# Kernel tuning notes

Hardware: AMD Instinct MI355X
Metric: run time of the kernel (lower is better)

The kernel has to match this reference:

```python
import jax, jax.numpy as jnp
import numpy as np

B, D, NH, HD = 32, 384, 8, 48
HP = WP = 14
N = HP * WP
L = 24
EPS_LN = 1e-5


def _ln(x, w, b):
    m = jnp.mean(x, -1, keepdims=True)
    v = jnp.mean((x - m) ** 2, -1, keepdims=True)
    return (x - m) * jax.lax.rsqrt(v + EPS_LN) * w + b


def _gelu(x):
    return jax.nn.gelu(x, approximate=False)


def _conv(x, w, s, p, groups=1):
    return jax.lax.conv_general_dilated(x, w, (s, s), [(p, p), (p, p)],
        dimension_numbers=('NCHW', 'OIHW', 'NCHW'), feature_group_count=groups)


def _bn(x, g, b):
    # eval-mode BatchNorm2d with running_mean=0, running_var=1
    scale = g * jax.lax.rsqrt(jnp.asarray(1.0 + 1e-5, x.dtype))
    return x * scale[None, :, None, None] + b[None, :, None, None]


def _pos_embed(pos_w, pos_b):
    two_pi = 2.0 * np.pi
    y = (jnp.arange(HP, dtype=jnp.float32) + 1.0) / ((HP + 1e-6) * two_pi)
    xg = (jnp.arange(WP, dtype=jnp.float32) + 1.0) / ((WP + 1e-6) * two_pi)
    y_embed = jnp.broadcast_to(y[:, None], (HP, WP))
    x_embed = jnp.broadcast_to(xg[None, :], (HP, WP))
    dim_t = 10000.0 ** (2.0 * (jnp.arange(32) // 2).astype(jnp.float32) / 32.0)
    px = x_embed[..., None] / dim_t  # [H,W,32]
    py = y_embed[..., None] / dim_t
    px = jnp.stack([jnp.sin(px[..., 0::2]), jnp.cos(px[..., 1::2])], -1).reshape(HP, WP, 32)
    py = jnp.stack([jnp.sin(py[..., 0::2]), jnp.cos(py[..., 1::2])], -1).reshape(HP, WP, 32)
    pos = jnp.concatenate([py, px], -1)  # [H,W,64]
    pos = jnp.einsum('hwc,dc->hwd', pos, pos_w[:, :, 0, 0]) + pos_b
    return pos.reshape(1, N, D)


def _xca_block(t, p):
    Bc = t.shape[0]
    h = _ln(t, p['n1_w'], p['n1_b'])
    qkv = (h @ p['qkv_w'].T + p['qkv_b']).reshape(Bc, N, 3, NH, HD)
    q = qkv[:, :, 0].transpose(0, 2, 3, 1)  # [B,H,d,N]
    k = qkv[:, :, 1].transpose(0, 2, 3, 1)
    v = qkv[:, :, 2].transpose(0, 2, 3, 1)
    q = q / jnp.maximum(jnp.linalg.norm(q, axis=-1, keepdims=True), 1e-12)
    k = k / jnp.maximum(jnp.linalg.norm(k, axis=-1, keepdims=True), 1e-12)
    attn = jnp.einsum('bhdn,bhen->bhde', q, k) * p['temp'][None, :, None, None]
    a = jax.nn.softmax(attn, -1)  # channel-wise softmax over d_h
    o = jnp.einsum('bhde,bhen->bnhd', a, v).reshape(Bc, N, D)
    o = o @ p['proj_w'].T + p['proj_b']
    t = t + p['g1'] * o
    h = _ln(t, p['n3_w'], p['n3_b']).transpose(0, 2, 1).reshape(Bc, D, HP, WP)
    h = _conv(h, p['lpi1_w'], 1, 1, groups=D) + p['lpi1_b'][None, :, None, None]
    h = _bn(_gelu(h), p['lpi_bn_g'], p['lpi_bn_b'])
    h = _conv(h, p['lpi2_w'], 1, 1, groups=D) + p['lpi2_b'][None, :, None, None]
    t = t + p['g3'] * h.reshape(Bc, D, N).transpose(0, 2, 1)
    h = _ln(t, p['n2_w'], p['n2_b'])
    h = _gelu(h @ p['fc1_w'].T + p['fc1_b']) @ p['fc2_w'].T + p['fc2_b']
    return t + p['g2'] * h


def _ca_block(t, p):
    Bc, Nc, _ = t.shape
    h = _ln(t, p['n1_w'], p['n1_b'])
    qkv = (h @ p['qkv_w'].T + p['qkv_b']).reshape(Bc, Nc, 3, NH, HD)
    q = qkv[:, :, 0].transpose(0, 2, 1, 3)  # [B,H,N,d]
    k = qkv[:, :, 1].transpose(0, 2, 1, 3)
    v = qkv[:, :, 2].transpose(0, 2, 1, 3)
    attn = jnp.sum(q[:, :, :1] * k, -1) * (HD ** -0.5)  # [B,H,N]
    a = jax.nn.softmax(attn, -1)
    cls = jnp.einsum('bhn,bhnd->bhd', a, v).reshape(Bc, 1, D)
    cls = cls @ p['proj_w'].T + p['proj_b']
    attn_out = jnp.concatenate([cls, h[:, 1:]], 1)
    t = t + p['g1'] * attn_out
    t = _ln(t, p['n2_w'], p['n2_b'])
    res = t
    cls2 = _gelu(t[:, :1] @ p['fc1_w'].T + p['fc1_b']) @ p['fc2_w'].T + p['fc2_b']
    return jnp.concatenate([p['g2'] * cls2, t[:, 1:]], 1) + res


def setup_inputs() -> dict:
    key = jax.random.key(0)
    k = iter(jax.random.split(key, 64))
    def rn(shape, std=0.02):
        return jax.random.normal(next(k), shape, jnp.float32) * std
    inp = {}
    inp['x'] = jax.random.normal(next(k), (B, 3, 224, 224), jnp.float32)
    inp['cls_token'] = rn((1, 1, D))
    inp['pos_w'] = rn((D, 64, 1, 1))
    inp['pos_b'] = jnp.zeros((D,))
    for i, (co, ci) in enumerate([(48, 3), (96, 48), (192, 96), (384, 192)], 1):
        inp['pe_w%d' % i] = rn((co, ci, 3, 3))
        inp['pe_g%d' % i] = jnp.ones((co,))
        inp['pe_b%d' % i] = jnp.zeros((co,))
    inp['xqkv_w'] = rn((L, 3 * D, D)); inp['xqkv_b'] = jnp.zeros((L, 3 * D))
    inp['xproj_w'] = rn((L, D, D)); inp['xproj_b'] = jnp.zeros((L, D))
    inp['xtemp'] = jnp.ones((L, NH))
    for n in ('n1', 'n2', 'n3'):
        inp['x%s_w' % n] = jnp.ones((L, D)); inp['x%s_b' % n] = jnp.zeros((L, D))
    inp['xfc1_w'] = rn((L, 4 * D, D)); inp['xfc1_b'] = jnp.zeros((L, 4 * D))
    inp['xfc2_w'] = rn((L, D, 4 * D)); inp['xfc2_b'] = jnp.zeros((L, D))
    inp['xlpi1_w'] = rn((L, D, 1, 3, 3), 0.1); inp['xlpi1_b'] = jnp.zeros((L, D))
    inp['xlpi2_w'] = rn((L, D, 1, 3, 3), 0.1); inp['xlpi2_b'] = jnp.zeros((L, D))
    inp['xbn_g'] = jnp.ones((L, D)); inp['xbn_b'] = jnp.zeros((L, D))
    for g in ('g1', 'g2', 'g3'):
        inp['x%s' % g] = jnp.full((L, D), 1e-5)
    L2 = 2
    inp['cqkv_w'] = rn((L2, 3 * D, D)); inp['cqkv_b'] = jnp.zeros((L2, 3 * D))
    inp['cproj_w'] = rn((L2, D, D)); inp['cproj_b'] = jnp.zeros((L2, D))
    for n in ('n1', 'n2'):
        inp['c%s_w' % n] = jnp.ones((L2, D)); inp['c%s_b' % n] = jnp.zeros((L2, D))
    inp['cfc1_w'] = rn((L2, 4 * D, D)); inp['cfc1_b'] = jnp.zeros((L2, 4 * D))
    inp['cfc2_w'] = rn((L2, D, 4 * D)); inp['cfc2_b'] = jnp.zeros((L2, D))
    inp['cg1'] = jnp.full((L2, D), 1e-5); inp['cg2'] = jnp.full((L2, D), 1e-5)
    inp['norm_w'] = jnp.ones((D,)); inp['norm_b'] = jnp.zeros((D,))
    inp['head_w'] = rn((1000, D)); inp['head_b'] = jnp.zeros((1000,))
    return inp


def reference(x, cls_token, pos_w, pos_b, pe_w1, pe_g1, pe_b1, pe_w2, pe_g2, pe_b2, pe_w3, pe_g3, pe_b3, pe_w4, pe_g4, pe_b4, xqkv_w, xqkv_b, xproj_w, xproj_b, xtemp, xn1_w, xn1_b, xn2_w, xn2_b, xn3_w, xn3_b, xfc1_w, xfc1_b, xfc2_w, xfc2_b, xlpi1_w, xlpi1_b, xlpi2_w, xlpi2_b, xbn_g, xbn_b, xg1, xg2, xg3, cqkv_w, cqkv_b, cproj_w, cproj_b, cn1_w, cn1_b, cn2_w, cn2_b, cfc1_w, cfc1_b, cfc2_w, cfc2_b, cg1, cg2, norm_w, norm_b, head_w, head_b):
    h = _gelu(_bn(_conv(x, pe_w1, 2, 1), pe_g1, pe_b1))
    h = _gelu(_bn(_conv(h, pe_w2, 2, 1), pe_g2, pe_b2))
    h = _gelu(_bn(_conv(h, pe_w3, 2, 1), pe_g3, pe_b3))
    h = _bn(_conv(h, pe_w4, 2, 1), pe_g4, pe_b4)  # [B,D,14,14]
    t = h.reshape(h.shape[0], D, N).transpose(0, 2, 1)  # [B,N,D]
    t = t + _pos_embed(pos_w, pos_b)
    xca = {'qkv_w': xqkv_w, 'qkv_b': xqkv_b, 'proj_w': xproj_w, 'proj_b': xproj_b,
           'temp': xtemp, 'n1_w': xn1_w, 'n1_b': xn1_b, 'n2_w': xn2_w, 'n2_b': xn2_b,
           'n3_w': xn3_w, 'n3_b': xn3_b, 'fc1_w': xfc1_w, 'fc1_b': xfc1_b,
           'fc2_w': xfc2_w, 'fc2_b': xfc2_b, 'lpi1_w': xlpi1_w, 'lpi1_b': xlpi1_b,
           'lpi2_w': xlpi2_w, 'lpi2_b': xlpi2_b, 'lpi_bn_g': xbn_g, 'lpi_bn_b': xbn_b,
           'g1': xg1, 'g2': xg2, 'g3': xg3}
    t, _ = jax.lax.scan(lambda c, p: (_xca_block(c, p), None), t, xca)
    t = jnp.concatenate([jnp.broadcast_to(cls_token, (t.shape[0], 1, D)), t], 1)
    for i in range(2):
        p = {'qkv_w': cqkv_w[i], 'qkv_b': cqkv_b[i], 'proj_w': cproj_w[i],
             'proj_b': cproj_b[i], 'n1_w': cn1_w[i], 'n1_b': cn1_b[i],
             'n2_w': cn2_w[i], 'n2_b': cn2_b[i], 'fc1_w': cfc1_w[i],
             'fc1_b': cfc1_b[i], 'fc2_w': cfc2_w[i], 'fc2_b': cfc2_b[i],
             'g1': cg1[i], 'g2': cg2[i]}
        t = _ca_block(t, p)
    t = _ln(t, norm_w, norm_b)[:, 0]
    return t @ head_w.T + head_b
```

## Files before the change

kernel.cpp:

```cpp
#include <hip/hip_runtime.h>
#include <hip/hip_bf16.h>

#define B_ 32
#define D_ 384
#define N_ 196
#define NH_ 8
#define HD_ 48
#define L_ 24

typedef __bf16 bf16x8 __attribute__((ext_vector_type(8)));
typedef float f32x4 __attribute__((ext_vector_type(4)));

__device__ __forceinline__ float gelu_f(float v){
    return 0.5f * v * (1.0f + erff(v * 0.70710678118654752f));
}

__global__ __launch_bounds__(256) void cvt_bf(const float* __restrict__ s, __bf16* __restrict__ d, long n){
    long i = ((long)blockIdx.x * 256 + threadIdx.x) * 8;
    if (i >= n) return;
    float4 a = *reinterpret_cast<const float4*>(s + i);
    float4 b = *reinterpret_cast<const float4*>(s + i + 4);
    bf16x8 r;
    r[0] = (__bf16)a.x; r[1] = (__bf16)a.y; r[2] = (__bf16)a.z; r[3] = (__bf16)a.w;
    r[4] = (__bf16)b.x; r[5] = (__bf16)b.y; r[6] = (__bf16)b.z; r[7] = (__bf16)b.w;
    *reinterpret_cast<bf16x8*>(d + i) = r;
}

__global__ __launch_bounds__(256) void cvt_pad(const float* __restrict__ s, __bf16* __restrict__ d,
                                               int rows, int K, int rows_pad){
    int id = blockIdx.x * 256 + threadIdx.x;
    if (id >= rows_pad * K) return;
    int r = id / K;
    d[id] = (r < rows) ? (__bf16)s[id] : (__bf16)0.f;
}

__global__ __launch_bounds__(256) void wprep(const float* __restrict__ w, __bf16* __restrict__ W2,
                                             int Co, int Ci, int Kpad){
    int id = blockIdx.x * 256 + threadIdx.x;
    if (id >= Co * Kpad) return;
    int co = id / Kpad, k = id - co * Kpad;
    float v = 0.f;
    if (k < 9 * Ci){
        int tap = k / Ci, ci = k - tap * Ci;
        v = w[((long)co * Ci + ci) * 9 + tap];
    }
    W2[id] = (__bf16)v;
}

__global__ __launch_bounds__(256) void im2col_x(const float* __restrict__ x, __bf16* __restrict__ A){
    int id = blockIdx.x * 256 + threadIdx.x;
    if (id >= 401408) return;
    int ox = id % 112; int t1 = id / 112; int oy = t1 % 112; int b = t1 / 112;
    __bf16 buf[32];
    #pragma unroll
    for (int i = 0; i < 32; i++) buf[i] = (__bf16)0.f;
    const float* xb = x + (long)b * 3 * 224 * 224;
    #pragma unroll
    for (int tap = 0; tap < 9; tap++){
        int ky = tap / 3, kx = tap % 3;
        int iy = oy * 2 - 1 + ky, ix = ox * 2 - 1 + kx;
        if ((unsigned)iy < 224u && (unsigned)ix < 224u){
            #pragma unroll
            for (int ci = 0; ci < 3; ci++)
                buf[tap * 3 + ci] = (__bf16)xb[((long)ci * 224 + iy) * 224 + ix];
        }
    }
    __bf16* dst = A + (long)id * 32;
    #pragma unroll
    for (int i = 0; i < 4; i++)
        *reinterpret_cast<bf16x8*>(dst + i * 8) = *reinterpret_cast<bf16x8*>(buf + i * 8);
}

__global__ __launch_bounds__(256) void im2col_bf(const __bf16* __restrict__ in, __bf16* __restrict__ A,
                                                 int C, int Hi, int Wi, int Ho, int Wo, int Kpad, int total){
    int id = blockIdx.x * 256 + threadIdx.x;
    if (id >= total) return;
    int tap = id % 9; int pix = id / 9;
    int ox = pix % Wo; int t1 = pix / Wo; int oy = t1 % Ho; int b = t1 / Ho;
    int ky = tap / 3, kx = tap % 3;
    int iy = oy * 2 - 1 + ky, ix = ox * 2 - 1 + kx;
    __bf16* dst = A + (long)pix * Kpad + tap * C;
    if ((unsigned)iy < (unsigned)Hi && (unsigned)ix < (unsigned)Wi){
        const __bf16* src = in + ((long)(b * Hi + iy) * Wi + ix) * C;
        for (int c = 0; c < C; c += 8)
            *reinterpret_cast<bf16x8*>(dst + c) = *reinterpret_cast<const bf16x8*>(src + c);
    } else {
        bf16x8 z{};
        for (int c = 0; c < C; c += 8) *reinterpret_cast<bf16x8*>(dst + c) = z;
    }
    if (tap == 0){
        bf16x8 z{};
        for (int c = 9 * C; c < Kpad; c += 8)
            *reinterpret_cast<bf16x8*>(A + (long)pix * Kpad + c) = z;
    }
}

template<int GELU, int POSOUT>
__global__ __launch_bounds__(256) void gemm_conv(const __bf16* __restrict__ A, int Kpad,
                                                 const __bf16* __restrict__ W,
                                                 const float* __restrict__ g, const float* __restrict__ bb,
                                                 void* __restrict__ Cv, int N,
                                                 const float* __restrict__ pos){
    __shared__ __align__(16) char smem[20480];
    char* Ab = smem;
    char* Bb = smem + 10240;
    const int tid  = threadIdx.x;
    const int lane = tid & 63;
    const int wn   = (tid >> 6) & 1;
    const int wm   = tid >> 7;
    const int row0 = blockIdx.x * 128;
    const int col0 = blockIdx.y * 128;
    const int hi = lane >> 4, lo = lane & 15;
    f32x4 acc[4][4] = {};
    auto loadA = [&](int kk, int i)->bf16x8 {
        int p = i * 256 + tid;
        int r = p >> 2, cq = p & 3;
        return *reinterpret_cast<const bf16x8*>(A + (long)(row0 + r) * Kpad + kk + cq * 8);
    };
    auto loadB = [&](int kk, int i)->bf16x8 {
        int p = i * 256 + tid;
        int r = p >> 2, cq = p & 3;
        int gc = col0 + r;
        bf16x8 vw{};
        if (gc < N) vw = *reinterpret_cast<const bf16x8*>(W + (long)gc * Kpad + kk + cq * 8);
        return vw;
    };
    bf16x8 vaC0 = loadA(0, 0), vaC1 = loadA(0, 1);
    bf16x8 vwC0 = loadB(0, 0), vwC1 = loadB(0, 1);
    for (int k0 = 0; k0 < Kpad; k0 += 32){
        #pragma unroll
        for (int i = 0; i < 2; i++){
            int p = i * 256 + tid;
            int r = p >> 2, cq = p & 3;
            *reinterpret_cast<bf16x8*>(Ab + r * 80 + cq * 16) = i ? vaC1 : vaC0;
            *reinterpret_cast<bf16x8*>(Bb + r * 80 + cq * 16) = i ? vwC1 : vwC0;
        }
        __syncthreads();
        int kn = (k0 + 32 < Kpad) ? k0 + 32 : k0;
        bf16x8 vaN0 = loadA(kn, 0), vaN1 = loadA(kn, 1);
        bf16x8 vwN0 = loadB(kn, 0), vwN1 = loadB(kn, 1);
        bf16x8 af[4], bfr[4];
        #pragma unroll
        for (int m = 0; m < 4; m++)
            af[m] = *reinterpret_cast<const bf16x8*>(Ab + (wm * 64 + m * 16 + lo) * 80 + hi * 16);
        #pragma unroll
        for (int n = 0; n < 4; n++)
            bfr[n] = *reinterpret_cast<const bf16x8*>(Bb + (wn * 64 + n * 16 + lo) * 80 + hi * 16);
        #pragma unroll
        for (int m = 0; m < 4; m++)
            #pragma unroll
            for (int n = 0; n < 4; n++)
                acc[m][n] = __builtin_amdgcn_mfma_f32_16x16x32_bf16(af[m], bfr[n], acc[m][n], 0, 0, 0);
        __syncthreads();
        vaC0 = vaN0; vaC1 = vaN1; vwC0 = vwN0; vwC1 = vwN1;
    }
    float* Cf = (float*)Cv;
    __bf16* Cb = (__bf16*)Cv;
    #pragma unroll
    for (int m = 0; m < 4; m++){
        #pragma unroll
        for (int n = 0; n < 4; n++){
            int row = row0 + wm * 64 + m * 16 + hi * 4;
            int col = col0 + wn * 64 + n * 16 + lo;
            if (col >= N) continue;
            float scale = g[col] * rsqrtf(1.0f + 1e-5f);
            float bv = bb[col];
            #pragma unroll
            for (int j = 0; j < 4; j++){
                float v = acc[m][n][j] * scale + bv;
                if (GELU) v = gelu_f(v);
                if (POSOUT)
                    Cf[(long)(row + j) * 384 + col] = v + pos[((row + j) % 196) * 384 + col];
                else
                    Cb[(long)(row + j) * N + col] = (__bf16)v;
            }
        }
    }
}

__global__ __launch_bounds__(128) void ln384(const float* __restrict__ x, long xstride,
                                             const float* __restrict__ w, const float* __restrict__ b,
                                             float* __restrict__ y, long ystride){
    long row = blockIdx.x;
    int tid = threadIdx.x;
    const float* xr = x + row * xstride;
    float v0 = xr[tid], v1 = xr[tid + 128], v2 = xr[tid + 256];
    float s = v0 + v1 + v2;
    float ss = v0 * v0 + v1 * v1 + v2 * v2;
    for (int off = 32; off; off >>= 1){ s += __shfl_down(s, off); ss += __shfl_down(ss, off); }
    __shared__ float rs[2], rss[2];
    if ((tid & 63) == 0){ rs[tid >> 6] = s; rss[tid >> 6] = ss; }
    __syncthreads();
    float S = rs[0] + rs[1], SS = rss[0] + rss[1];
    float m = S * (1.0f / 384.0f);
    float var = SS * (1.0f / 384.0f) - m * m;
    float r = rsqrtf(var + 1e-5f);
    float* yr = y + row * ystride;
    yr[tid]       = (v0 - m) * r * w[tid]       + b[tid];
    yr[tid + 128] = (v1 - m) * r * w[tid + 128] + b[tid + 128];
    yr[tid + 256] = (v2 - m) * r * w[tid + 256] + b[tid + 256];
}

__global__ __launch_bounds__(128) void ln384_bf(const float* __restrict__ x,
                                                const float* __restrict__ w, const float* __restrict__ b,
                                                __bf16* __restrict__ y){
    long row = blockIdx.x;
    int tid = threadIdx.x;
    const float* xr = x + row * 384;
    float v0 = xr[tid], v1 = xr[tid + 128], v2 = xr[tid + 256];
    float s = v0 + v1 + v2;
    float ss = v0 * v0 + v1 * v1 + v2 * v2;
    for (int off = 32; off; off >>= 1){ s += __shfl_down(s, off); ss += __shfl_down(ss, off); }
    __shared__ float rs[2], rss[2];
    if ((tid & 63) == 0){ rs[tid >> 6] = s; rss[tid >> 6] = ss; }
    __syncthreads();
    float S = rs[0] + rs[1], SS = rss[0] + rss[1];
    float m = S * (1.0f / 384.0f);
    float var = SS * (1.0f / 384.0f) - m * m;
    float r = rsqrtf(var + 1e-5f);
    __bf16* yr = y + row * 384;
    yr[tid]       = (__bf16)((v0 - m) * r * w[tid]       + b[tid]);
    yr[tid + 128] = (__bf16)((v1 - m) * r * w[tid + 128] + b[tid + 128]);
    yr[tid + 256] = (__bf16)((v2 - m) * r * w[tid + 256] + b[tid + 256]);
}

__global__ __launch_bounds__(128) void proj_red_lnt(const float* __restrict__ pp,
                                                    const float* __restrict__ pbias,
                                                    const float* __restrict__ g1,
                                                    float* __restrict__ t,
                                                    const float* __restrict__ n3w, const float* __restrict__ n3b,
                                                    float* __restrict__ ht){
    long row = blockIdx.x;
    int tid = threadIdx.x;
    const long MT = 6272L * 384;
    float v[3];
    #pragma unroll
    for (int i = 0; i < 3; i++){
        int c = tid + i * 128;
        long idx = row * 384 + c;
        float sacc = pp[idx] + pp[MT + idx] + pbias[c];
        v[i] = t[idx] + g1[c] * sacc;
        t[idx] = v[i];
    }
    float s = v[0] + v[1] + v[2];
    float ss = v[0] * v[0] + v[1] * v[1] + v[2] * v[2];
    for (int off = 32; off; off >>= 1){ s += __shfl_down(s, off); ss += __shfl_down(ss, off); }
    __shared__ float rs[2], rss[2];
    if ((tid & 63) == 0){ rs[tid >> 6] = s; rss[tid >> 6] = ss; }
    __syncthreads();
    float S = rs[0] + rs[1], SS = rss[0] + rss[1];
    float m = S * (1.0f / 384.0f);
    float var = SS * (1.0f / 384.0f) - m * m;
    float r = rsqrtf(var + 1e-5f);
    int b = (int)(row / 196), n = (int)(row % 196);
    float* yb = ht + ((long)b * 384) * 196 + n;
    #pragma unroll
    for (int i = 0; i < 3; i++){
        int c = tid + i * 128;
        yb[(long)c * 196] = (v[i] - m) * r * n3w[c] + n3b[c];
    }
}

__global__ __launch_bounds__(128) void fc2_red_ln(const float* __restrict__ pp,
                                                  const float* __restrict__ fbias,
                                                  const float* __restrict__ g2,
                                                  float* __restrict__ t,
                                                  const float* __restrict__ n1w, const float* __restrict__ n1b,
                                                  __bf16* __restrict__ h){
    long row = blockIdx.x;
    int tid = threadIdx.x;
    const long MT = 6272L * 384;
    float v[3];
    #pragma unroll
    for (int i = 0; i < 3; i++){
        int c = tid + i * 128;
        long idx = row * 384 + c;
        float sacc = pp[idx] + pp[MT + idx] + pp[2 * MT + idx] + fbias[c];
        v[i] = t[idx] + g2[c] * sacc;
        t[idx] = v[i];
    }
    float s = v[0] + v[1] + v[2];
    float ss = v[0] * v[0] + v[1] * v[1] + v[2] * v[2];
    for (int off = 32; off; off >>= 1){ s += __shfl_down(s, off); ss += __shfl_down(ss, off); }
    __shared__ float rs[2], rss[2];
    if ((tid & 63) == 0){ rs[tid >> 6] = s; rss[tid >> 6] = ss; }
    __syncthreads();
    float S = rs[0] + rs[1], SS = rss[0] + rss[1];
    float m = S * (1.0f / 384.0f);
    float var = SS * (1.0f / 384.0f) - m * m;
    float r = rsqrtf(var + 1e-5f);
    __bf16* yr = h + row * 384;
    #pragma unroll
    for (int i = 0; i < 3; i++){
        int c = tid + i * 128;
        yr[c] = (__bf16)((v[i] - m) * r * n1w[c] + n1b[c]);
    }
}

template<int MODE, int OUTBF, int ACVT, int GUARD, int SPLITK, int NGUARD>
__global__ __launch_bounds__(256) void gemm_bb2(const void* __restrict__ Av, long lda,
                                                const __bf16* __restrict__ W, int Kw,
                                                const float* __restrict__ bias,
                                                void* __restrict__ Cv, long ldc,
                                                int K, int M, int Ncols){
    __shared__ __align__(16) char smem[15360];
    char* Ab = smem;
    char* Bb = smem + 5120;
    const int tid = threadIdx.x;
    const int lane = tid & 63;
    const int wn = tid >> 6;
    const int row0 = blockIdx.x * 64;
    const int col0 = blockIdx.y * 128;
    const int hi = lane >> 4, lo = lane & 15;
    const int kbase = SPLITK ? blockIdx.z * K : 0;
    const __bf16* Abf = (const __bf16*)Av;
    const float* Af = (const float*)Av;
    const int r_a = tid >> 2, cq_a = tid & 3;
    f32x4 acc[4][2] = {};
    auto loadA = [&](int kk)->bf16x8 {
        bf16x8 va{};
        int grow = row0 + r_a;
        if (!GUARD || grow < M){
            long ai = (long)grow * lda + kk + cq_a * 8;
            if (ACVT){
                float4 a0 = *reinterpret_cast<const float4*>(Af + ai);
                float4 a1 = *reinterpret_cast<const float4*>(Af + ai + 4);
                va[0] = (__bf16)a0.x; va[1] = (__bf16)a0.y; va[2] = (__bf16)a0.z; va[3] = (__bf16)a0.w;
                va[4] = (__bf16)a1.x; va[5] = (__bf16)a1.y; va[6] = (__bf16)a1.z; va[7] = (__bf16)a1.w;
            } else {
                va = *reinterpret_cast<const bf16x8*>(Abf + ai);
            }
        }
        return va;
    };
    auto loadB = [&](int kk, int i)->bf16x8 {
        int p = i * 256 + tid;
        int r = p >> 2, cq = p & 3;
        return *reinterpret_cast<const bf16x8*>(W + (long)(col0 + r) * Kw + kk + cq * 8);
    };
    bf16x8 vaC = loadA(kbase);
    bf16x8 vwC0 = loadB(kbase, 0), vwC1 = loadB(kbase, 1);
    for (int k0 = 0; k0 < K; k0 += 32){
        *reinterpret_cast<bf16x8*>(Ab + r_a * 80 + cq_a * 16) = vaC;
        #pragma unroll
        for (int i = 0; i < 2; i++){
            int p = i * 256 + tid;
            int r = p >> 2, cq = p & 3;
            *reinterpret_cast<bf16x8*>(Bb + r * 80 + cq * 16) = i ? vwC1 : vwC0;
        }
        __syncthreads();
        int kn = kbase + ((k0 + 32 < K) ? k0 + 32 : k0);
        bf16x8 vaN = loadA(kn);
        bf16x8 vwN0 = loadB(kn, 0), vwN1 = loadB(kn, 1);
        bf16x8 af[4], bfr[2];
        #pragma unroll
        for (int m = 0; m < 4; m++)
            af[m] = *reinterpret_cast<const bf16x8*>(Ab + (m * 16 + lo) * 80 + hi * 16);
        #pragma unroll
        for (int n = 0; n < 2; n++)
            bfr[n] = *reinterpret_cast<const bf16x8*>(Bb + (wn * 32 + n * 16 + lo) * 80 + hi * 16);
        #pragma unroll
        for (int m = 0; m < 4; m++)
            #pragma unroll
            for (int n = 0; n < 2; n++)
                acc[m][n] = __builtin_amdgcn_mfma_f32_16x16x32_bf16(af[m], bfr[n], acc[m][n], 0, 0, 0);
        __syncthreads();
        vaC = vaN; vwC0 = vwN0; vwC1 = vwN1;
    }
    float* Cf = (float*)Cv;
    __bf16* Cb = (__bf16*)Cv;
    if (SPLITK) Cf += (long)blockIdx.z * M * ldc;
    #pragma unroll
    for (int m = 0; m < 4; m++){
        #pragma unroll
        for (int n = 0; n < 2; n++){
            int row = row0 + m * 16 + hi * 4;
            int col = col0 + wn * 32 + n * 16 + lo;
            if (NGUARD && col >= Ncols) continue;
            float bv = (MODE == 3) ? 0.f : bias[col];
            #pragma unroll
            for (int j = 0; j < 4; j++){
                if (GUARD && (row + j) >= M) continue;
                float v = acc[m][n][j] + bv;
                if (MODE == 1) v = gelu_f(v);
                long ci = (long)(row + j) * ldc + col;
                if (OUTBF) Cb[ci] = (__bf16)v;
                else Cf[ci] = v;
            }
        }
    }
}

__global__ __launch_bounds__(384) void pos_embed(const float* __restrict__ pw, const float* __restrict__ pb,
                                                 float* __restrict__ pos){
    __shared__ float p64[64];
    int n = blockIdx.x;
    int iy = n / 14, ix = n % 14;
    int t = threadIdx.x;
    if (t < 64){
        int axis = t >> 5;
        int c = t & 31;
        int u = c >> 1;
        float coord = (axis == 0) ? (float)(iy + 1) : (float)(ix + 1);
        float val = coord / ((14.0f + 1e-6f) * 6.283185307179586f);
        float T = powf(10000.0f, (float)u / 16.0f);
        float a = val / T;
        p64[t] = (c & 1) ? cosf(a) : sinf(a);
    }
    __syncthreads();
    float acc = 0.f;
    const float* wr = pw + (long)t * 64;
    #pragma unroll 8
    for (int c = 0; c < 64; c++) acc += p64[c] * wr[c];
    pos[n * 384 + t] = acc + pb[t];
}

__global__ __launch_bounds__(256) void xca2(const __bf16* __restrict__ qkv, const float* __restrict__ temp,
                                            __bf16* __restrict__ o){
    __shared__ __align__(16) char smem[74880];
    __bf16* qs = (__bf16*)smem;
    __bf16* ks = (__bf16*)(smem + 22272);
    __bf16* vt = (__bf16*)(smem + 44544);
    float* inq = (float*)(smem + 74496);
    float* ink = (float*)(smem + 74688);
    float* att = (float*)smem;
    __bf16* abf = (__bf16*)(smem + 22272);
    int bh = blockIdx.x;
    int b = bh >> 3, h = bh & 7;
    const int tid = threadIdx.x;
    const int wid = tid >> 6, lane = tid & 63;
    const int hi = lane >> 4, lo = lane & 15;
    const __bf16* base = qkv + ((long)b * 196) * 1152 + h * 48;
    bf16x8 z8 = {};
    for (int idx = tid; idx < 48 * 28; idx += 256){
        int d = idx / 28, n = 196 + idx % 28;
        qs[d * 232 + n] = (__bf16)0.f;
        ks[d * 232 + n] = (__bf16)0.f;
    }
    for (int idx = tid; idx < 208 * 2; idx += 256){
        int n = idx >> 1, c = 48 + (idx & 1) * 8;
        *reinterpret_cast<bf16x8*>(vt + n * 72 + c) = z8;
    }
    for (int ch = tid; ch < 196 * 6; ch += 256){
        int n = ch / 6, c = ch % 6, d0 = c * 8;
        bf16x8 q8 = *reinterpret_cast<const bf16x8*>(base + (long)n * 1152 + d0);
        bf16x8 k8 = *reinterpret_cast<const bf16x8*>(base + (long)n * 1152 + 384 + d0);
        #pragma unroll
        for (int j = 0; j < 8; j++){
            qs[(d0 + j) * 232 + n] = q8[j];
            ks[(d0 + j) * 232 + n] = k8[j];
        }
        bf16x8 v8 = *reinterpret_cast<const bf16x8*>(base + (long)n * 1152 + 768 + d0);
        *reinterpret_cast<bf16x8*>(vt + n * 72 + d0) = v8;
    }
    __syncthreads();
    for (int r = wid; r < 48; r += 4){
        float sq = 0.f, sk = 0.f;
        for (int n = lane; n < 196; n += 64){
            float qv = (float)qs[r * 232 + n];
            float kv = (float)ks[r * 232 + n];
            sq += qv * qv; sk += kv * kv;
        }
        for (int off = 32; off; off >>= 1){ sq += __shfl_down(sq, off); sk += __shfl_down(sk, off); }
        if (lane == 0){
            inq[r] = 1.0f / fmaxf(sqrtf(sq), 1e-12f);
            ink[r] = 1.0f / fmaxf(sqrtf(sk), 1e-12f);
        }
    }
    __syncthreads();
    float tempv = temp[h];
    f32x4 qk0 = {}, qk1 = {}, qk2 = {};
    __builtin_amdgcn_s_setprio(1);
    {
        int mi = wid / 3, ni = wid % 3;
        #pragma unroll
        for (int k0 = 0; k0 < 224; k0 += 32){
            bf16x8 af = *reinterpret_cast<const bf16x8*>(qs + (mi * 16 + lo) * 232 + k0 + hi * 8);
            bf16x8 bf = *reinterpret_cast<const bf16x8*>(ks + (ni * 16 + lo) * 232 + k0 + hi * 8);
            qk0 = __builtin_amdgcn_mfma_f32_16x16x32_bf16(af, bf, qk0, 0, 0, 0);
        }
    }
    {
        int tt = wid + 4;
        int mi = tt / 3, ni = tt % 3;
        #pragma unroll
        for (int k0 = 0; k0 < 224; k0 += 32){
            bf16x8 af = *reinterpret_cast<const bf16x8*>(qs + (mi * 16 + lo) * 232 + k0 + hi * 8);
            bf16x8 bf = *reinterpret_cast<const bf16x8*>(ks + (ni * 16 + lo) * 232 + k0 + hi * 8);
            qk1 = __builtin_amdgcn_mfma_f32_16x16x32_bf16(af, bf, qk1, 0, 0, 0);
        }
    }
    if (wid == 0){
        int mi = 2, ni = 2;
        #pragma unroll
        for (int k0 = 0; k0 < 224; k0 += 32){
            bf16x8 af = *reinterpret_cast<const bf16x8*>(qs + (mi * 16 + lo) * 232 + k0 + hi * 8);
            bf16x8 bf = *reinterpret_cast<const bf16x8*>(ks + (ni * 16 + lo) * 232 + k0 + hi * 8);
            qk2 = __builtin_amdgcn_mfma_f32_16x16x32_bf16(af, bf, qk2, 0, 0, 0);
        }
    }
    __builtin_amdgcn_s_setprio(0);
    __syncthreads();
    {
        int mi = wid / 3, ni = wid % 3;
        int e = ni * 16 + lo;
        float se = ink[e] * tempv;
        #pragma unroll
        for (int j = 0; j < 4; j++){
            int d = mi * 16 + hi * 4 + j;
            att[d * 68 + e] = qk0[j] * inq[d] * se;
        }
    }
    {
        int tt = wid + 4;
        int mi = tt / 3, ni = tt % 3;
        int e = ni * 16 + lo;
        float se = ink[e] * tempv;
        #pragma unroll
        for (int j = 0; j < 4; j++){
            int d = mi * 16 + hi * 4 + j;
            att[d * 68 + e] = qk1[j] * inq[d] * se;
        }
    }
    if (wid == 0){
        int e = 2 * 16 + lo;
        float se = ink[e] * tempv;
        #pragma unroll
        for (int j = 0; j < 4; j++){
            int d = 2 * 16 + hi * 4 + j;
            att[d * 68 + e] = qk2[j] * inq[d] * se;
        }
    }
    __syncthreads();
    if (tid < 192){
        int r = tid >> 2, q4 = tid & 3;
        const float* row = att + r * 68 + q4 * 12;
        float mx = -1e30f;
        #pragma unroll
        for (int i = 0; i < 12; i++) mx = fmaxf(mx, row[i]);
        mx = fmaxf(mx, __shfl_xor(mx, 1));
        mx = fmaxf(mx, __shfl_xor(mx, 2));
        float pv[12]; float sm = 0.f;
        #pragma unroll
        for (int i = 0; i < 12; i++){ pv[i] = expf(row[i] - mx); sm += pv[i]; }
        sm += __shfl_xor(sm, 1);
        sm += __shfl_xor(sm, 2);
        float inv = 1.0f / sm;
        #pragma unroll
        for (int i = 0; i < 12; i++) abf[r * 72 + q4 * 12 + i] = (__bf16)(pv[i] * inv);
    }
    for (int idx = tid; idx < 48 * 3; idx += 256){
        int r = idx / 3, c = 48 + (idx % 3) * 8;
        *reinterpret_cast<bf16x8*>(abf + r * 72 + c) = z8;
    }
    __syncthreads();
    __bf16* ob = o + ((long)b * 196) * 384 + h * 48;
    __builtin_amdgcn_s_setprio(1);
    for (int tt = wid; tt < 39; tt += 4){
        int mi = tt / 13, ni = tt % 13;
        f32x4 acc = {};
        #pragma unroll
        for (int e0 = 0; e0 < 64; e0 += 32){
            bf16x8 af = *reinterpret_cast<const bf16x8*>(abf + (mi * 16 + lo) * 72 + e0 + hi * 8);
            bf16x8 bf = *reinterpret_cast<const bf16x8*>(vt + (ni * 16 + lo) * 72 + e0 + hi * 8);
            acc = __builtin_amdgcn_mfma_f32_16x16x32_bf16(af, bf, acc, 0, 0, 0);
        }
        int n = ni * 16 + lo;
        if (n < 196){
            #pragma unroll
            for (int j = 0; j < 4; j++){
                int d = mi * 16 + hi * 4 + j;
                ob[(long)n * 384 + d] = (__bf16)acc[j];
            }
        }
    }
    __builtin_amdgcn_s_setprio(0);
}

__global__ __launch_bounds__(256) void lpi(const float* __restrict__ ht,
                                           const float* __restrict__ w1, const float* __restrict__ b1,
                                           const float* __restrict__ bng, const float* __restrict__ bnb,
                                           const float* __restrict__ w2, const float* __restrict__ b2,
                                           const float* __restrict__ g3, float* __restrict__ t){
    int bd = blockIdx.x;
    int d = bd % 384, b = bd / 384;
    __shared__ float p[16][16];
    __shared__ float p2[16][16];
    __shared__ float wA[9], wB[9];
    int tt = threadIdx.x;
    int yy = tt / 16, xx = tt % 16;
    p[yy][xx] = 0.f; p2[yy][xx] = 0.f;
    if (tt < 9){ wA[tt] = w1[d * 9 + tt]; wB[tt] = w2[d * 9 + tt]; }
    __syncthreads();
    if (tt < 196){
        int y = tt / 14, x = tt % 14;
        p[y + 1][x + 1] = ht[((long)b * 384 + d) * 196 + tt];
    }
    __syncthreads();
    if (tt < 196){
        int y = tt / 14, x = tt % 14;
        float a = 0.f;
        #pragma unroll
        for (int ky = 0; ky < 3; ky++)
            #pragma unroll
            for (int kx = 0; kx < 3; kx++)
                a += wA[ky * 3 + kx] * p[y + ky][x + kx];
        a += b1[d];
        a = gelu_f(a);
        a = a * (bng[d] * rsqrtf(1.0f + 1e-5f)) + bnb[d];
        p2[y + 1][x + 1] = a;
    }
    __syncthreads();
    if (tt < 196){
        int y = tt / 14, x = tt % 14;
        float a = 0.f;
        #pragma unroll
        for (int ky = 0; ky < 3; ky++)
            #pragma unroll
            for (int kx = 0; kx < 3; kx++)
                a += wB[ky * 3 + kx] * p2[y + ky][x + kx];
        a += b2[d];
        long ti = ((long)b * 196 + tt) * 384 + d;
        t[ti] += g3[d] * a;
    }
}

__global__ __launch_bounds__(256) void concat_cls(const float* __restrict__ t, const float* __restrict__ clstok,
                                                  float* __restrict__ tc){
    long i = (long)blockIdx.x * 256 + threadIdx.x;
    if (i >= (long)B_ * 197 * 384) return;
    int d = (int)(i % 384);
    long bn = i / 384;
    int n = (int)(bn % 197);
    int b = (int)(bn / 197);
    tc[i] = (n == 0) ? clstok[d] : t[((long)b * 196 + (n - 1)) * 384 + d];
}

__global__ __launch_bounds__(256) void ca_attn(const __bf16* __restrict__ qkv, float* __restrict__ clsp){
    int bh = blockIdx.x;
    int b = bh >> 3, h = bh & 7;
    const __bf16* base = qkv + (long)b * 197 * 1152 + h * 48;
    __shared__ float q0[48];
    __shared__ float at2[197];
    __shared__ float smax, ssum;
    int tid = threadIdx.x;
    if (tid < 48) q0[tid] = (float)base[tid];
    __syncthreads();
    if (tid < 197){
        const __bf16* kr = base + (long)tid * 1152 + 384;
        float s = 0.f;
        for (int d = 0; d < 48; d++) s += q0[d] * (float)kr[d];
        at2[tid] = s * rsqrtf(48.0f);
    }
    __syncthreads();
    if (tid == 0){
        float m = -1e30f;
        for (int n = 0; n < 197; n++) m = fmaxf(m, at2[n]);
        smax = m;
    }
    __syncthreads();
    if (tid < 197) at2[tid] = expf(at2[tid] - smax);
    __syncthreads();
    if (tid == 0){
        float s = 0.f;
        for (int n = 0; n < 197; n++) s += at2[n];
        ssum = s;
    }
    __syncthreads();
    if (tid < 48){
        const __bf16* vb = base + 768 + tid;
        float s = 0.f;
        for (int n = 0; n < 197; n++) s += at2[n] * (float)vb[(long)n * 1152];
        clsp[b * 384 + h * 48 + tid] = s / ssum;
    }
}

__global__ __launch_bounds__(256) void ca_update1(const float* __restrict__ clso, const float* __restrict__ hc,
                                                  const float* __restrict__ g1, float* __restrict__ tc){
    long i = (long)blockIdx.x * 256 + threadIdx.x;
    if (i >= (long)B_ * 197 * 384) return;
    int d = (int)(i % 384);
    long bn = i / 384;
    int n = (int)(bn % 197);
    int b = (int)(bn / 197);
    float add = (n == 0) ? clso[b * 384 + d] : hc[i];
    tc[i] += g1[d] * add;
}

__global__ __launch_bounds__(256) void ca_update2(const float* __restrict__ cls2, const float* __restrict__ hc,
                                                  const float* __restrict__ g2, float* __restrict__ tc){
    long i = (long)blockIdx.x * 256 + threadIdx.x;
    if (i >= (long)B_ * 197 * 384) return;
    int d = (int)(i % 384);
    long bn = i / 384;
    int n = (int)(bn % 197);
    int b = (int)(bn / 197);
    float hv = hc[i];
    tc[i] = (n == 0) ? (g2[d] * cls2[b * 384 + d] + hv) : (hv + hv);
}

extern "C" void kernel_launch(void* const* d_in, const int* in_sizes, int n_in,
                              void* d_out, int out_size, void* d_ws, size_t ws_size,
                              hipStream_t stream){
    (void)in_sizes; (void)n_in; (void)out_size; (void)ws_size;
    const float* x      = (const float*)d_in[0];
    const float* clstok = (const float*)d_in[1];
    const float* pos_w  = (const float*)d_in[2];
    const float* pos_b  = (const float*)d_in[3];
    const float* pe_w[4] = {(const float*)d_in[4], (const float*)d_in[7], (const float*)d_in[10], (const float*)d_in[13]};
    const float* pe_g[4] = {(const float*)d_in[5], (const float*)d_in[8], (const float*)d_in[11], (const float*)d_in[14]};
    const float* pe_b[4] = {(const float*)d_in[6], (const float*)d_in[9], (const float*)d_in[12], (const float*)d_in[15]};
    const float* xqkv_w = (const float*)d_in[16];
    const float* xqkv_b = (const float*)d_in[17];
    const float* xproj_w = (const float*)d_in[18];
    const float* xproj_b = (const float*)d_in[19];
    const float* xtemp  = (const float*)d_in[20];
    const float* xn1_w = (const float*)d_in[21];
    const float* xn1_b = (const float*)d_in[22];
    const float* xn2_w = (const float*)d_in[23];
    const float* xn2_b = (const float*)d_in[24];
    const float* xn3_w = (const float*)d_in[25];
    const float* xn3_b = (const float*)d_in[26];
    const float* xfc1_w = (const float*)d_in[27];
    const float* xfc1_b = (const float*)d_in[28];
    const float* xfc2_w = (const float*)d_in[29];
    const float* xfc2_b = (const float*)d_in[30];
    const float* xlpi1_w = (const float*)d_in[31];
    const float* xlpi1_b = (const float*)d_in[32];
    const float* xlpi2_w = (const float*)d_in[33];
    const float* xlpi2_b = (const float*)d_in[34];
    const float* xbn_g = (const float*)d_in[35];
    const float* xbn_b = (const float*)d_in[36];
    const float* xg1 = (const float*)d_in[37];
    const float* xg2 = (const float*)d_in[38];
    const float* xg3 = (const float*)d_in[39];
    const float* cqkv_w = (const float*)d_in[40];
    const float* cqkv_b = (const float*)d_in[41];
    const float* cproj_w = (const float*)d_in[42];
    const float* cproj_b = (const float*)d_in[43];
    const float* cn1_w = (const float*)d_in[44];
    const float* cn1_b = (const float*)d_in[45];
    const float* cn2_w = (const float*)d_in[46];
    const float* cn2_b = (const float*)d_in[47];
    const float* cfc1_w = (const float*)d_in[48];
    const float* cfc1_b = (const float*)d_in[49];
    const float* cfc2_w = (const float*)d_in[50];
    const float* cfc2_b = (const float*)d_in[51];
    const float* cg1 = (const float*)d_in[52];
    const float* cg2 = (const float*)d_in[53];
    const float* norm_w = (const float*)d_in[54];
    const float* norm_b = (const float*)d_in[55];
    const float* head_w = (const float*)d_in[56];
    const float* head_b = (const float*)d_in[57];
    float* outp = (float*)d_out;

    float* ws = (float*)d_ws;
    __bf16* A1   = (__bf16*)(ws);
    __bf16* A2   = (__bf16*)(ws);
    __bf16* A3   = (__bf16*)(ws);
    __bf16* A4   = (__bf16*)(ws);
    __bf16* out1 = (__bf16*)(ws + 22500000L);
    __bf16* out2 = (__bf16*)(ws + 22500000L);
    __bf16* out3 = (__bf16*)(ws + 27400000L);
    __bf16* wcv  = (__bf16*)(ws + 36000000L);
    __bf16* W1c = wcv;
    __bf16* W2c = wcv + 1536;
    __bf16* W3c = wcv + 44544;
    __bf16* W4c = wcv + 216576;
    __bf16* wqkv_bf = (__bf16*)(ws);
    __bf16* wproj_bf = (__bf16*)(ws + 5308416L);
    __bf16* wfc1_bf = (__bf16*)(ws + 7077888L);
    __bf16* wfc2_bf = (__bf16*)(ws + 14155776L);
    float*  t       = ws + 21233664L;
    float*  pos     = ws + 23642112L;
    __bf16* h_bf    = (__bf16*)(ws + 23717376L);
    __bf16* qkv_bf  = (__bf16*)(ws + 24921600L);
    __bf16* o_bf    = (__bf16*)(ws + 28534272L);
    float*  ht      = ws + 29738496L;
    __bf16* f1_bf   = (__bf16*)(ws + 32146944L);
    float*  pproj   = ws + 32146944L;
    float*  pfc2    = ws + 24921600L;
    float* tc   = ws;
    float* hc   = ws + 2420736L;
    __bf16* qkvc_bf = (__bf16*)(ws + 4841472L);
    float* clsp = ws + 8472576L;
    float* clso = clsp + 12288;
    float* f1c  = clso + 12288;
    float* cls2 = f1c + 49152;
    float* clsf = cls2 + 12288;
    __bf16* cqkv_bf  = (__bf16*)(ws + 9000000L);
    __bf16* cproj_bf = (__bf16*)(ws + 9500000L);
    __bf16* cfc1_bf  = (__bf16*)(ws + 9800000L);
    __bf16* cfc2_bf  = (__bf16*)(ws + 10400000L);
    __bf16* headw_bf = (__bf16*)(ws + 11000000L);

    wprep<<<(48 * 32 + 255) / 256, 256, 0, stream>>>(pe_w[0], W1c, 48, 3, 32);
    wprep<<<(96 * 448 + 255) / 256, 256, 0, stream>>>(pe_w[1], W2c, 96, 48, 448);
    wprep<<<(192 * 896 + 255) / 256, 256, 0, stream>>>(pe_w[2], W3c, 192, 96, 896);
    wprep<<<(384 * 1728 + 255) / 256, 256, 0, stream>>>(pe_w[3], W4c, 384, 192, 1728);

    im2col_x<<<1568, 256, 0, stream>>>(x, A1);
    { dim3 g(3136, 1); gemm_conv<1, 0><<<g, 256, 0, stream>>>(A1, 32, W1c, pe_g[0], pe_b[0], out1, 48, nullptr); }
    im2col_bf<<<(100352 * 9 + 255) / 256, 256, 0, stream>>>(out1, A2, 48, 112, 112, 56, 56, 448, 100352 * 9);
    { dim3 g(784, 1); gemm_conv<1, 0><<<g, 256, 0, stream>>>(A2, 448, W2c, pe_g[1], pe_b[1], out2, 96, nullptr); }
    im2col_bf<<<(25088 * 9 + 255) / 256, 256, 0, stream>>>(out2, A3, 96, 56, 56, 28, 28, 896, 25088 * 9);
    pos_embed<<<196, 384, 0, stream>>>(pos_w, pos_b, pos);
    { dim3 g(196, 2); gemm_conv<1, 0><<<g, 256, 0, stream>>>(A3, 896, W3c, pe_g[2], pe_b[2], out3, 192, nullptr); }
    im2col_bf<<<(6272 * 9 + 255) / 256, 256, 0, stream>>>(out3, A4, 192, 28, 28, 14, 14, 1728, 6272 * 9);
    { dim3 g(49, 3); gemm_conv<0, 1><<<g, 256, 0, stream>>>(A4, 1728, W4c, pe_g[3], pe_b[3], t, 384, pos); }

    {
        long n1 = (long)L_ * 1152 * 384;
        long n2 = (long)L_ * 384 * 384;
        long n3 = (long)L_ * 1536 * 384;
        cvt_bf<<<(int)((n1 + 2047) / 2048), 256, 0, stream>>>(xqkv_w, wqkv_bf, n1);
        cvt_bf<<<(int)((n2 + 2047) / 2048), 256, 0, stream>>>(xproj_w, wproj_bf, n2);
        cvt_bf<<<(int)((n3 + 2047) / 2048), 256, 0, stream>>>(xfc1_w, wfc1_bf, n3);
        cvt_bf<<<(int)((n3 + 2047) / 2048), 256, 0, stream>>>(xfc2_w, wfc2_bf, n3);
    }

    const int M = B_ * N_;
    ln384_bf<<<M, 128, 0, stream>>>(t, xn1_w, xn1_b, h_bf);
    for (int l = 0; l < L_; l++){
        {
            dim3 g(98, 9);
            gemm_bb2<0, 1, 0, 0, 0, 0><<<g, 256, 0, stream>>>(h_bf, 384, wqkv_bf + (long)l * 1152 * 384, 384,
                                                              xqkv_b + l * 1152, qkv_bf, 1152, 384, M, 0);
        }
        xca2<<<B_ * NH_, 256, 0, stream>>>(qkv_bf, xtemp + l * 8, o_bf);
        {
            dim3 g(98, 3, 2);
            gemm_bb2<3, 0, 0, 0, 1, 0><<<g, 256, 0, stream>>>(o_bf, 384, wproj_bf + (long)l * 384 * 384, 384,
                                                              nullptr, pproj, 384, 192, M, 0);
        }
        proj_red_lnt<<<M, 128, 0, stream>>>(pproj, xproj_b + l * 384, xg1 + l * 384, t,
                                            xn3_w + l * 384, xn3_b + l * 384, ht);
        lpi<<<B_ * D_, 256, 0, stream>>>(ht, xlpi1_w + (long)l * 384 * 9, xlpi1_b + l * 384,
                                         xbn_g + l * 384, xbn_b + l * 384,
                                         xlpi2_w + (long)l * 384 * 9, xlpi2_b + l * 384,
                                         xg3 + l * 384, t);
        ln384_bf<<<M, 128, 0, stream>>>(t, xn2_w + l * 384, xn2_b + l * 384, h_bf);
        {
            dim3 g(98, 12);
            gemm_bb2<1, 1, 0, 0, 0, 0><<<g, 256, 0, stream>>>(h_bf, 384, wfc1_bf + (long)l * 1536 * 384, 384,
                                                              xfc1_b + l * 1536, f1_bf, 1536, 384, M, 0);
        }
        {
            dim3 g(98, 3, 3);
            gemm_bb2<3, 0, 0, 0, 1, 0><<<g, 256, 0, stream>>>(f1_bf, 1536, wfc2_bf + (long)l * 1536 * 384, 1536,
                                                              nullptr, pfc2, 384, 512, M, 0);
        }
        int ln = (l + 1) % L_;
        fc2_red_ln<<<M, 128, 0, stream>>>(pfc2, xfc2_b + l * 384, xg2 + l * 384, t,
                                          xn1_w + ln * 384, xn1_b + ln * 384, h_bf);
    }

    const long NC = (long)B_ * 197 * 384;
    concat_cls<<<(int)(NC / 256), 256, 0, stream>>>(t, clstok, tc);
    {
        long nc = (long)2 * 1152 * 384;
        cvt_bf<<<(int)((nc + 2047) / 2048), 256, 0, stream>>>(cqkv_w, cqkv_bf, nc);
        long np = (long)2 * 384 * 384;
        cvt_bf<<<(int)((np + 2047) / 2048), 256, 0, stream>>>(cproj_w, cproj_bf, np);
        long nf = (long)2 * 1536 * 384;
        cvt_bf<<<(int)((nf + 2047) / 2048), 256, 0, stream>>>(cfc1_w, cfc1_bf, nf);
        cvt_bf<<<(int)((nf + 2047) / 2048), 256, 0, stream>>>(cfc2_w, cfc2_bf, nf);
        cvt_pad<<<(1024 * 384 + 255) / 256, 256, 0, stream>>>(head_w, headw_bf, 1000, 384, 1024);
    }
    const int MC = B_ * 197;
    for (int i = 0; i < 2; i++){
        ln384<<<MC, 128, 0, stream>>>(tc, 384, cn1_w + i * 384, cn1_b + i * 384, hc, 384);
        {
            dim3 g(99, 9);
            gemm_bb2<0, 1, 1, 1, 0, 0><<<g, 256, 0, stream>>>(hc, 384, cqkv_bf + (long)i * 1152 * 384, 384,
                                                              cqkv_b + i * 1152, qkvc_bf, 1152, 384, MC, 0);
        }
        ca_attn<<<B_ * NH_, 256, 0, stream>>>(qkvc_bf, clsp);
        {
            dim3 g(1, 3);
            gemm_bb2<0, 0, 1, 1, 0, 0><<<g, 256, 0, stream>>>(clsp, 384, cproj_bf + (long)i * 384 * 384, 384,
                                                              cproj_b + i * 384, clso, 384, 384, 32, 0);
        }
        ca_update1<<<(int)(NC / 256), 256, 0, stream>>>(clso, hc, cg1 + i * 384, tc);
        ln384<<<MC, 128, 0, stream>>>(tc, 384, cn2_w + i * 384, cn2_b + i * 384, hc, 384);
        {
            dim3 g(1, 12);
            gemm_bb2<1, 0, 1, 1, 0, 0><<<g, 256, 0, stream>>>(hc, (long)197 * 384, cfc1_bf + (long)i * 1536 * 384, 384,
                                                              cfc1_b + i * 1536, f1c, 1536, 384, 32, 0);
        }
        {
            dim3 g(1, 3);
            gemm_bb2<0, 0, 1, 1, 0, 0><<<g, 256, 0, stream>>>(f1c, 1536, cfc2_bf + (long)i * 1536 * 384, 1536,
                                                              cfc2_b + i * 384, cls2, 384, 1536, 32, 0);
        }
        ca_update2<<<(int)(NC / 256), 256, 0, stream>>>(cls2, hc, cg2 + i * 384, tc);
    }

    ln384<<<32, 128, 0, stream>>>(tc, (long)197 * 384, norm_w, norm_b, clsf, 384);
    {
        dim3 g(1, 8);
        gemm_bb2<0, 0, 1, 1, 0, 1><<<g, 256, 0, stream>>>(clsf, 384, headw_bf, 384,
                                                          head_b, outp, 1000, 384, 32, 1000);
    }
}
```

Measured before the change: 4.589 ms.

## Replace split-K fp32 partials with 64x64 bf16 GEMM and bf16 residual buffers

Swaps the split-K proj and fc2 GEMMs, which wrote fp32 partial sums that a reduction kernel then combined, for a new small-tile 64x64 GEMM that runs the full K loop and writes bias-added bf16 output. The LPI kernel now writes its scaled output to a bf16 buffer instead of doing a read-modify-write on t. The separate LN kernel is replaced by a fused residual-add plus LN. This cuts fp32 partial-sum traffic and extra passes over memory, at the cost of bf16 rounding on the residual branch and less parallelism in K per GEMM block.

```diff
diff --git a/kernel.cpp b/kernel.cpp
--- a/kernel.cpp
+++ b/kernel.cpp
@@ -224,22 +224,19 @@
     yr[tid + 256] = (__bf16)((v2 - m) * r * w[tid + 256] + b[tid + 256]);
 }
 
-__global__ __launch_bounds__(128) void proj_red_lnt(const float* __restrict__ pp,
-                                                    const float* __restrict__ pbias,
+__global__ __launch_bounds__(128) void proj_res_lnt(const __bf16* __restrict__ o2,
                                                     const float* __restrict__ g1,
                                                     float* __restrict__ t,
                                                     const float* __restrict__ n3w, const float* __restrict__ n3b,
                                                     float* __restrict__ ht){
     long row = blockIdx.x;
     int tid = threadIdx.x;
-    const long MT = 6272L * 384;
     float v[3];
     #pragma unroll
     for (int i = 0; i < 3; i++){
         int c = tid + i * 128;
         long idx = row * 384 + c;
-        float sacc = pp[idx] + pp[MT + idx] + pbias[c];
-        v[i] = t[idx] + g1[c] * sacc;
+        v[i] = t[idx] + g1[c] * (float)o2[idx];
         t[idx] = v[i];
     }
     float s = v[0] + v[1] + v[2];
@@ -261,22 +258,51 @@
     }
 }
 
-__global__ __launch_bounds__(128) void fc2_red_ln(const float* __restrict__ pp,
-                                                  const float* __restrict__ fbias,
+__global__ __launch_bounds__(128) void ln2res(float* __restrict__ t,
+                                              const __bf16* __restrict__ hadd,
+                                              const float* __restrict__ n2w, const float* __restrict__ n2b,
+                                              __bf16* __restrict__ h){
+    long row = blockIdx.x;
+    int tid = threadIdx.x;
+    float v[3];
+    #pragma unroll
+    for (int i = 0; i < 3; i++){
+        int c = tid + i * 128;
+        long idx = row * 384 + c;
+        v[i] = t[idx] + (float)hadd[idx];
+        t[idx] = v[i];
+    }
+    float s = v[0] + v[1] + v[2];
+    float ss = v[0] * v[0] + v[1] * v[1] + v[2] * v[2];
+    for (int off = 32; off; off >>= 1){ s += __shfl_down(s, off); ss += __shfl_down(ss, off); }
+    __shared__ float rs[2], rss[2];
+    if ((tid & 63) == 0){ rs[tid >> 6] = s; rss[tid >> 6] = ss; }
+    __syncthreads();
+    float S = rs[0] + rs[1], SS = rss[0] + rss[1];
+    float m = S * (1.0f / 384.0f);
+    float var = SS * (1.0f / 384.0f) - m * m;
+    float r = rsqrtf(var + 1e-5f);
+    __bf16* yr = h + row * 384;
+    #pragma unroll
+    for (int i = 0; i < 3; i++){
+        int c = tid + i * 128;
+        yr[c] = (__bf16)((v[i] - m) * r * n2w[c] + n2b[c]);
+    }
+}
+
+__global__ __launch_bounds__(128) void fc2_res_ln(const __bf16* __restrict__ f2,
                                                   const float* __restrict__ g2,
                                                   float* __restrict__ t,
                                                   const float* __restrict__ n1w, const float* __restrict__ n1b,
                                                   __bf16* __restrict__ h){
     long row = blockIdx.x;
     int tid = threadIdx.x;
-    const long MT = 6272L * 384;
     float v[3];
     #pragma unroll
     for (int i = 0; i < 3; i++){
         int c = tid + i * 128;
         long idx = row * 384 + c;
-        float sacc = pp[idx] + pp[MT + idx] + pp[2 * MT + idx] + fbias[c];
-        v[i] = t[idx] + g2[c] * sacc;
+        v[i] = t[idx] + g2[c] * (float)f2[idx];
         t[idx] = v[i];
     }
     float s = v[0] + v[1] + v[2];
@@ -391,6 +417,59 @@
     }
 }
 
+__global__ __launch_bounds__(256) void gemm_bb3(const __bf16* __restrict__ A, long lda,
+                                                const __bf16* __restrict__ W, int Kw,
+                                                const float* __restrict__ bias,
+                                                __bf16* __restrict__ C, long ldc,
+                                                int K){
+    __shared__ __align__(16) char smem[10240];
+    char* Ab = smem;
+    char* Bb = smem + 5120;
+    const int tid = threadIdx.x;
+    const int lane = tid & 63;
+    const int wn = tid >> 6;
+    const int row0 = blockIdx.x * 64;
+    const int col0 = blockIdx.y * 64;
+    const int hi = lane >> 4, lo = lane & 15;
+    const int r_s = tid >> 2, cq_s = tid & 3;
+    f32x4 acc[4] = {};
+    auto loadA = [&](int kk)->bf16x8 {
+        return *reinterpret_cast<const bf16x8*>(A + (long)(row0 + r_s) * lda + kk + cq_s * 8);
+    };
+    auto loadB = [&](int kk)->bf16x8 {
+        return *reinterpret_cast<const bf16x8*>(W + (long)(col0 + r_s) * Kw + kk + cq_s * 8);
+    };
+    bf16x8 vaC = loadA(0);
+    bf16x8 vwC = loadB(0);
+    for (int k0 = 0; k0 < K; k0 += 32){
+        *reinterpret_cast<bf16x8*>(Ab + r_s * 80 + cq_s * 16) = vaC;
+        *reinterpret_cast<bf16x8*>(Bb + r_s * 80 + cq_s * 16) = vwC;
+        __syncthreads();
+        int kn = (k0 + 32 < K) ? k0 + 32 : k0;
+        bf16x8 vaN = loadA(kn);
+        bf16x8 vwN = loadB(kn);
+        bf16x8 af[4], bfr;
+        #pragma unroll
+        for (int m = 0; m < 4; m++)
+            af[m] = *reinterpret_cast<const bf16x8*>(Ab + (m * 16 + lo) * 80 + hi * 16);
+        bfr = *reinterpret_cast<const bf16x8*>(Bb + (wn * 16 + lo) * 80 + hi * 16);
+        #pragma unroll
+        for (int m = 0; m < 4; m++)
+            acc[m] = __builtin_amdgcn_mfma_f32_16x16x32_bf16(af[m], bfr, acc[m], 0, 0, 0);
+        __syncthreads();
+        vaC = vaN; vwC = vwN;
+    }
+    #pragma unroll
+    for (int m = 0; m < 4; m++){
+        int row = row0 + m * 16 + hi * 4;
+        int col = col0 + wn * 16 + lo;
+        float bv = bias[col];
+        #pragma unroll
+        for (int j = 0; j < 4; j++)
+            C[(long)(row + j) * ldc + col] = (__bf16)(acc[m][j] + bv);
+    }
+}
+
 __global__ __launch_bounds__(384) void pos_embed(const float* __restrict__ pw, const float* __restrict__ pb,
                                                  float* __restrict__ pos){
     __shared__ float p64[64];
@@ -491,11 +570,10 @@
         }
     }
     if (wid == 0){
-        int mi = 2, ni = 2;
         #pragma unroll
         for (int k0 = 0; k0 < 224; k0 += 32){
-            bf16x8 af = *reinterpret_cast<const bf16x8*>(qs + (mi * 16 + lo) * 232 + k0 + hi * 8);
-            bf16x8 bf = *reinterpret_cast<const bf16x8*>(ks + (ni * 16 + lo) * 232 + k0 + hi * 8);
+            bf16x8 af = *reinterpret_cast<const bf16x8*>(qs + (2 * 16 + lo) * 232 + k0 + hi * 8);
+            bf16x8 bf = *reinterpret_cast<const bf16x8*>(ks + (2 * 16 + lo) * 232 + k0 + hi * 8);
             qk2 = __builtin_amdgcn_mfma_f32_16x16x32_bf16(af, bf, qk2, 0, 0, 0);
         }
     }
@@ -577,11 +655,11 @@
     __builtin_amdgcn_s_setprio(0);
 }
 
-__global__ __launch_bounds__(256) void lpi(const float* __restrict__ ht,
-                                           const float* __restrict__ w1, const float* __restrict__ b1,
-                                           const float* __restrict__ bng, const float* __restrict__ bnb,
-                                           const float* __restrict__ w2, const float* __restrict__ b2,
-                                           const float* __restrict__ g3, float* __restrict__ t){
+__global__ __launch_bounds__(256) void lpi_g(const float* __restrict__ ht,
+                                             const float* __restrict__ w1, const float* __restrict__ b1,
+                                             const float* __restrict__ bng, const float* __restrict__ bnb,
+                                             const float* __restrict__ w2, const float* __restrict__ b2,
+                                             const float* __restrict__ g3, __bf16* __restrict__ hadd){
     int bd = blockIdx.x;
     int d = bd % 384, b = bd / 384;
     __shared__ float p[16][16];
@@ -620,8 +698,7 @@
             for (int kx = 0; kx < 3; kx++)
                 a += wB[ky * 3 + kx] * p2[y + ky][x + kx];
         a += b2[d];
-        long ti = ((long)b * 196 + tt) * 384 + d;
-        t[ti] += g3[d] * a;
+        hadd[((long)b * 196 + tt) * 384 + d] = (__bf16)(g3[d] * a);
     }
 }
 
@@ -778,8 +855,9 @@
     __bf16* o_bf    = (__bf16*)(ws + 28534272L);
     float*  ht      = ws + 29738496L;
     __bf16* f1_bf   = (__bf16*)(ws + 32146944L);
-    float*  pproj   = ws + 32146944L;
-    float*  pfc2    = ws + 24921600L;
+    __bf16* o2_bf   = (__bf16*)(ws + 34555392L);
+    __bf16* f2_bf   = (__bf16*)(ws + 24921600L);
+    __bf16* hadd_bf = (__bf16*)(ws + 28534272L);
     float* tc   = ws;
     float* hc   = ws + 2420736L;
     __bf16* qkvc_bf = (__bf16*)(ws + 4841472L);
@@ -829,29 +907,29 @@
         }
         xca2<<<B_ * NH_, 256, 0, stream>>>(qkv_bf, xtemp + l * 8, o_bf);
         {
-            dim3 g(98, 3, 2);
-            gemm_bb2<3, 0, 0, 0, 1, 0><<<g, 256, 0, stream>>>(o_bf, 384, wproj_bf + (long)l * 384 * 384, 384,
-                                                              nullptr, pproj, 384, 192, M, 0);
-        }
-        proj_red_lnt<<<M, 128, 0, stream>>>(pproj, xproj_b + l * 384, xg1 + l * 384, t,
+            dim3 g(98, 6);
+            gemm_bb3<<<g, 256, 0, stream>>>(o_bf, 384, wproj_bf + (long)l * 384 * 384, 384,
+                                            xproj_b + l * 384, o2_bf, 384, 384);
+        }
+        proj_res_lnt<<<M, 128, 0, stream>>>(o2_bf, xg1 + l * 384, t,
                                             xn3_w + l * 384, xn3_b + l * 384, ht);
-        lpi<<<B_ * D_, 256, 0, stream>>>(ht, xlpi1_w + (long)l * 384 * 9, xlpi1_b + l * 384,
-                                         xbn_g + l * 384, xbn_b + l * 384,
-                                         xlpi2_w + (long)l * 384 * 9, xlpi2_b + l * 384,
-                                         xg3 + l * 384, t);
-        ln384_bf<<<M, 128, 0, stream>>>(t, xn2_w + l * 384, xn2_b + l * 384, h_bf);
+        lpi_g<<<B_ * D_, 256, 0, stream>>>(ht, xlpi1_w + (long)l * 384 * 9, xlpi1_b + l * 384,
+                                           xbn_g + l * 384, xbn_b + l * 384,
+                                           xlpi2_w + (long)l * 384 * 9, xlpi2_b + l * 384,
+                                           xg3 + l * 384, hadd_bf);
+        ln2res<<<M, 128, 0, stream>>>(t, hadd_bf, xn2_w + l * 384, xn2_b + l * 384, h_bf);
         {
             dim3 g(98, 12);
             gemm_bb2<1, 1, 0, 0, 0, 0><<<g, 256, 0, stream>>>(h_bf, 384, wfc1_bf + (long)l * 1536 * 384, 384,
                                                               xfc1_b + l * 1536, f1_bf, 1536, 384, M, 0);
         }
         {
-            dim3 g(98, 3, 3);
-            gemm_bb2<3, 0, 0, 0, 1, 0><<<g, 256, 0, stream>>>(f1_bf, 1536, wfc2_bf + (long)l * 1536 * 384, 1536,
-                                                              nullptr, pfc2, 384, 512, M, 0);
+            dim3 g(98, 6);
+            gemm_bb3<<<g, 256, 0, stream>>>(f1_bf, 1536, wfc2_bf + (long)l * 1536 * 384, 1536,
+                                            xfc2_b + l * 384, f2_bf, 384, 1536);
         }
         int ln = (l + 1) % L_;
-        fc2_red_ln<<<M, 128, 0, stream>>>(pfc2, xfc2_b + l * 384, xg2 + l * 384, t,
+        fc2_res_ln<<<M, 128, 0, stream>>>(f2_bf, xg2 + l * 384, t,
                                           xn1_w + ln * 384, xn1_b + ln * 384, h_bf);
     }
 
```

Result: faster. 4.188 ms (-8.7%).
